# Performance work log

Hardware: AMD Instinct MI355X
Metric: run time of the kernel (lower is better)

## Reference

```python
import jax, jax.numpy as jnp
import numpy as np

N_ROWS = 8192
EMBED = 256


def setup_inputs() -> dict:
    key = jax.random.key(0)
    k1, k2, k3, k4, k5 = jax.random.split(key, 5)
    M = jax.random.normal(k1, (N_ROWS, EMBED), dtype=jnp.float32)
    N = jax.random.normal(k2, (N_ROWS, EMBED), dtype=jnp.float32)
    gate_w_weight = jax.random.normal(k3, (1, EMBED), dtype=jnp.float32) * (1.0 / np.sqrt(EMBED))
    gate_w_bias = jax.random.normal(k4, (1,), dtype=jnp.float32)
    gate_b = jax.random.normal(k5, (1,), dtype=jnp.float32)
    return {"M": M, "N": N, "gate_w_weight": gate_w_weight,
            "gate_w_bias": gate_w_bias, "gate_b": gate_b}


def reference(M, N, gate_w_weight, gate_w_bias, gate_b):
    # scores: [n, n] = N @ M^T
    mt = jnp.matmul(N, M.T)
    # zero the diagonal (mt - diag(diag(mt)))
    n = mt.shape[0]
    idx = jnp.arange(n)
    diag_zeroed = mt.at[idx, idx].set(0.0)
    attn = jax.nn.softmax(diag_zeroed, axis=-1)
    out_attn = jnp.matmul(attn, M)  # [n, d]
    # gate: Linear(d -> 1) + extra scalar bias, then sigmoid
    gate_tmp = jnp.matmul(out_attn, gate_w_weight.T) + gate_w_bias + gate_b  # [n, 1]
    gate = jax.nn.sigmoid(gate_tmp)
    boosted = out_attn * gate + N * (1.0 - gate)
    return boosted[:, None, None, :]  # [n, 1, 1, d]
```

## Files before the change

### kernel.cpp

```cpp
#include <hip/hip_runtime.h>
#include <math.h>

#define NR   8192
#define DIM  256
#define QBLK 32

using f32x4  = __attribute__((ext_vector_type(4))) float;
using s4v    = __attribute__((ext_vector_type(4))) short;
using s8v    = __attribute__((ext_vector_type(8))) short;
using bf16x8 = __attribute__((ext_vector_type(8))) short;
typedef _Float16 f16x8 __attribute__((ext_vector_type(8)));
typedef _Float16 f16x4 __attribute__((ext_vector_type(4)));

__device__ __forceinline__ short f2bf(float x){
  union{float f; unsigned u;} v; v.f = x;
  unsigned r = v.u + 0x7fffu + ((v.u >> 16) & 1u);
  return (short)(r >> 16);
}
__device__ __forceinline__ float bf2f(short s){
  union{unsigned u; float f;} v; v.u = ((unsigned)(unsigned short)s) << 16;
  return v.f;
}
__device__ __forceinline__ short f2h(float x){
  union{_Float16 h; short s;} c; c.h = (_Float16)x; return c.s;
}

#define SS_SHORTS 32768
#define WS_BYTES_NEEDED (128u * 32768u * 2u)

#define LDS6_SHORTS 65536

__device__ __forceinline__ void dma16(const short* g, short* l){
  __builtin_amdgcn_global_load_lds(
      (const __attribute__((address_space(1))) unsigned int*)g,
      (__attribute__((address_space(3))) unsigned int*)l, 16, 0, 0);
}

__launch_bounds__(256)
__global__ void precompute_ws(const float* __restrict__ Mp, short* __restrict__ ws)
{
  const int tid = threadIdx.x;
  const int bx  = blockIdx.x;
  const int ss  = bx >> 4;
  const int sub = bx & 15;
  const int fi  = sub*256 + tid;
  const int plane = fi >> 11;
  const int rest  = fi & 2047;
  const int p   = rest >> 10;
  const int cl  = rest & 1023;
  const int ch  = cl >> 6;
  const int l   = cl & 63;
  const int li  = l & 15, g = l >> 4;

  short v[8];
  if (plane == 0){
    const int kk = ch >> 1, n = ch & 1;
    const int row = ss*64 + p*32 + n*16 + li;
    const int d0  = kk*32 + g*8;
    const float* src = Mp + (size_t)row*DIM + d0;
    #pragma unroll
    for (int j = 0; j < 8; ++j) v[j] = f2h(src[j]);
  } else {
    const int u   = p*16 + ch;
    const int par = u >> 3;
    const int np  = u & 7;
    #pragma unroll
    for (int j = 0; j < 8; ++j){
      const int nf = 2*np + (j >> 2);
      const int jj = j & 3;
      const int row = ss*64 + par*16 + (l >> 4)*4 + jj;
      const int col = nf*16 + (l & 15);
      v[j] = f2h(Mp[(size_t)row*DIM + col]);
    }
  }
  s8v ov = {v[0],v[1],v[2],v[3],v[4],v[5],v[6],v[7]};
  *(s8v*)(ws + (size_t)ss*SS_SHORTS + plane*16384 + p*8192 + ch*512 + l*8) = ov;
}

__launch_bounds__(512, 2)
__global__ void attn_gate_v9(const float* __restrict__ Np,
                             const float* __restrict__ gw, const float* __restrict__ gwb,
                             const float* __restrict__ gb,
                             const short* __restrict__ ws, float* __restrict__ out)
{
  extern __shared__ short S_[];
  const int tid  = threadIdx.x;
  const int w    = tid >> 6;
  const int lane = tid & 63;
  const int g    = lane >> 4;
  const int li   = lane & 15;
  const int qsub = w & 1;
  const int par  = w >> 1;
  const int qb   = blockIdx.x * QBLK;
  const int fbase = w * 8;
  const int fadd  = (w < 4) ? 0 : 16384;

  f16x8 qh[8];
  {
    const float* qrow = Np + (size_t)(qb + qsub*16 + li) * DIM;
    #pragma unroll
    for (int kk = 0; kk < 8; ++kk){
      const int d0 = kk*32 + g*8;
      #pragma unroll
      for (int j = 0; j < 8; ++j)
        qh[kk][j] = (_Float16)qrow[d0 + j];
    }
  }

  f32x4 o[16];
  #pragma unroll
  for (int nf = 0; nf < 16; ++nf){ f32x4 z = {0.f,0.f,0.f,0.f}; o[nf] = z; }
  float m0 = -1e30f, l0 = 0.0f;

  const int p2 = par >> 1, n2 = par & 1;
  const int kfrag_off = p2*8192 + n2*512 + lane*8;

  #pragma unroll
  for (int i = 0; i < 8; ++i){
    const int f = fbase + i;
    dma16(ws + (size_t)f*512 + lane*8, S_ + f*512 + fadd);
  }
  __syncthreads();

  for (int ss = 0; ss < 128; ++ss){
    const size_t ssb = (size_t)ss * SS_SHORTS;
    const int cur = (ss & 1) * 16384;

    if (ss < 127){
      const int nxt = 16384 - cur;
      const size_t nsb = ssb + SS_SHORTS;
      #pragma unroll
      for (int i = 0; i < 8; ++i){
        const int f = fbase + i;
        dma16(ws + nsb + (size_t)f*512 + lane*8, S_ + f*512 + nxt + fadd);
      }
    }

    f32x4 sa0, sa1, sa2, sa3;
    { f32x4 z = {0.f,0.f,0.f,0.f}; sa0 = z; sa1 = z; sa2 = z; sa3 = z; }
    {
      const short* kbase = S_ + cur + kfrag_off;
      __builtin_amdgcn_s_setprio(1);
      #pragma unroll
      for (int kk = 0; kk < 2; ++kk){
        f16x8 bh = *(const f16x8*)(kbase + kk*1024);
        sa0 = __builtin_amdgcn_mfma_f32_16x16x32_f16(bh, qh[kk], sa0, 0, 0, 0);
      }
      #pragma unroll
      for (int kk = 2; kk < 4; ++kk){
        f16x8 bh = *(const f16x8*)(kbase + kk*1024);
        sa1 = __builtin_amdgcn_mfma_f32_16x16x32_f16(bh, qh[kk], sa1, 0, 0, 0);
      }
      #pragma unroll
      for (int kk = 4; kk < 6; ++kk){
        f16x8 bh = *(const f16x8*)(kbase + kk*1024);
        sa2 = __builtin_amdgcn_mfma_f32_16x16x32_f16(bh, qh[kk], sa2, 0, 0, 0);
      }
      #pragma unroll
      for (int kk = 6; kk < 8; ++kk){
        f16x8 bh = *(const f16x8*)(kbase + kk*1024);
        sa3 = __builtin_amdgcn_mfma_f32_16x16x32_f16(bh, qh[kk], sa3, 0, 0, 0);
      }
      __builtin_amdgcn_s_setprio(0);
    }

    const int kvb = ss*64 + par*16 + g*4;
    const int qg  = qb + qsub*16 + li;
    float s_[4];
    #pragma unroll
    for (int i = 0; i < 4; ++i){
      float sv = (sa0[i] + sa1[i]) + (sa2[i] + sa3[i]);
      if (kvb + i == qg) sv = 0.0f;
      s_[i] = sv;
    }
    const float lmax = fmaxf(fmaxf(s_[0], s_[1]), fmaxf(s_[2], s_[3]));
    float sc = 1.0f;
    if (__any((int)(lmax > m0 + 8.0f))){
      float t = lmax;
      t = fmaxf(t, __shfl_xor(t, 16));
      t = fmaxf(t, __shfl_xor(t, 32));
      const float mn = fmaxf(m0, t);
      sc = __expf(m0 - mn);
      m0 = mn;
      float scr[4];
      #pragma unroll
      for (int i = 0; i < 4; ++i) scr[i] = __shfl(sc, g*4 + i);
      #pragma unroll
      for (int nf = 0; nf < 16; ++nf)
        #pragma unroll
        for (int i = 0; i < 4; ++i) o[nf][i] *= scr[i];
    }

    float p_[4];
    #pragma unroll
    for (int i = 0; i < 4; ++i) p_[i] = __expf(s_[i] - m0);

    f16x4 pa4;
    pa4[0] = (_Float16)p_[0]; pa4[1] = (_Float16)p_[1];
    pa4[2] = (_Float16)p_[2]; pa4[3] = (_Float16)p_[3];
    {
      const short* vbase = S_ + 32768 + cur + par*4096 + lane*8;
      __builtin_amdgcn_s_setprio(1);
      #pragma unroll
      for (int np = 0; np < 8; ++np){
        f16x8 v8 = *(const f16x8*)(vbase + np*512);
        f16x4 lo = __builtin_shufflevector(v8, v8, 0, 1, 2, 3);
        f16x4 hi = __builtin_shufflevector(v8, v8, 4, 5, 6, 7);
        o[2*np]   = __builtin_amdgcn_mfma_f32_16x16x16f16(pa4, lo, o[2*np],   0, 0, 0);
        o[2*np+1] = __builtin_amdgcn_mfma_f32_16x16x16f16(pa4, hi, o[2*np+1], 0, 0, 0);
      }
      __builtin_amdgcn_s_setprio(0);
    }

    float ps = (p_[0] + p_[1]) + (p_[2] + p_[3]);
    ps += __shfl_xor(ps, 16);
    ps += __shfl_xor(ps, 32);
    l0 = l0*sc + ps;

    __syncthreads();
  }

  float mr[4], lr[4];
  #pragma unroll
  for (int i = 0; i < 4; ++i){
    mr[i] = __shfl(m0, g*4 + i);
    lr[i] = __shfl(l0, g*4 + i);
  }

  float* dump = (float*)S_;
  if (par > 0){
    float* dp = dump + (size_t)((par-1)*128 + qsub*64 + lane) * 72;
    #pragma unroll
    for (int i = 0; i < 4; ++i){ dp[i] = mr[i]; dp[4+i] = lr[i]; }
    #pragma unroll
    for (int nf = 0; nf < 16; ++nf)
      #pragma unroll
      for (int i = 0; i < 4; ++i) dp[8 + nf*4 + i] = o[nf][i];
  }
  __syncthreads();
  if (par == 0){
    #pragma unroll
    for (int pp = 0; pp < 3; ++pp){
      const float* dp = dump + (size_t)(pp*128 + qsub*64 + lane) * 72;
      float a[4], b[4];
      #pragma unroll
      for (int i = 0; i < 4; ++i){
        float mb = dp[i], lb = dp[4+i];
        float mm = fmaxf(mr[i], mb);
        a[i] = __expf(mr[i] - mm);
        b[i] = __expf(mb - mm);
        lr[i] = lr[i]*a[i] + lb*b[i];
        mr[i] = mm;
      }
      #pragma unroll
      for (int nf = 0; nf < 16; ++nf)
        #pragma unroll
        for (int i = 0; i < 4; ++i)
          o[nf][i] = o[nf][i]*a[i] + dp[8 + nf*4 + i]*b[i];
    }

    float inv[4];
    #pragma unroll
    for (int i = 0; i < 4; ++i) inv[i] = 1.0f / lr[i];
    #pragma unroll
    for (int nf = 0; nf < 16; ++nf)
      #pragma unroll
      for (int i = 0; i < 4; ++i) o[nf][i] *= inv[i];

    float acc[4] = {0.f, 0.f, 0.f, 0.f};
    #pragma unroll
    for (int nf = 0; nf < 16; ++nf){
      float wv = gw[nf*16 + li];
      #pragma unroll
      for (int i = 0; i < 4; ++i) acc[i] += o[nf][i] * wv;
    }
    const float bias = gwb[0] + gb[0];
    float gt[4];
    #pragma unroll
    for (int i = 0; i < 4; ++i){
      float x = acc[i];
      x += __shfl_xor(x, 1);
      x += __shfl_xor(x, 2);
      x += __shfl_xor(x, 4);
      x += __shfl_xor(x, 8);
      gt[i] = 1.0f / (1.0f + __expf(-(x + bias)));
    }
    #pragma unroll
    for (int i = 0; i < 4; ++i){
      const int grow = qb + qsub*16 + g*4 + i;
      const float* nrow = Np + (size_t)grow * DIM;
      float* orow = out + (size_t)grow * DIM;
      #pragma unroll
      for (int nf = 0; nf < 16; ++nf){
        const int col = nf*16 + li;
        float nv = nrow[col];
        orow[col] = o[nf][i]*gt[i] + nv*(1.0f - gt[i]);
      }
    }
  }
}

#define KH0 0
#define KH1 8448
#define KL0 16896
#define KL1 25344
#define MT0 33792
#define MT1 44032
#define PBO 54272
#define LDS0_SHORTS 56832

__launch_bounds__(256, 1)
__global__ void attn_gate_v0(const float* __restrict__ Mp, const float* __restrict__ Np,
                             const float* __restrict__ gw, const float* __restrict__ gwb,
                             const float* __restrict__ gb, float* __restrict__ out)
{
  extern __shared__ short S_[];
  const int tid  = threadIdx.x;
  const int w    = tid >> 6;
  const int lane = tid & 63;
  const int g    = lane >> 4;
  const int li   = lane & 15;
  const int qsub = w & 1;
  const int par  = w >> 1;
  const int qb   = blockIdx.x * QBLK;

  short* khp = S_ + (par ? KH1 : KH0);
  short* klp = S_ + (par ? KL1 : KL0);
  short* mtp = S_ + (par ? MT1 : MT0);
  short* pb  = S_ + PBO + w * 640;

  bf16x8 qh[8], ql[8];
  {
    const float* qrow = Np + (size_t)(qb + qsub*16 + li) * DIM;
    #pragma unroll
    for (int kk = 0; kk < 8; ++kk){
      const int d0 = kk*32 + g*8;
      #pragma unroll
      for (int j = 0; j < 8; ++j){
        float f = qrow[d0 + j];
        short h = f2bf(f);
        qh[kk][j] = h;
        ql[kk][j] = f2bf(f - bf2f(h));
      }
    }
  }

  f32x4 o[16];
  #pragma unroll
  for (int nf = 0; nf < 16; ++nf){ f32x4 z = {0.f,0.f,0.f,0.f}; o[nf] = z; }
  float m0[4], l0[4];
  #pragma unroll
  for (int i = 0; i < 4; ++i){ m0[i] = -1e30f; l0[i] = 0.0f; }

  const int NSS = NR / 64;
  for (int ss = 0; ss < NSS; ++ss){
    {
      const int r  = tid >> 2;
      const int cb = (tid & 3) << 6;
      const int p  = r >> 5;
      const int rr = r & 31;
      short* kh = S_ + (p ? KH1 : KH0) + rr*264 + cb;
      short* kl = S_ + (p ? KL1 : KL0) + rr*264 + cb;
      short* mt = S_ + (p ? MT1 : MT0) + rr;
      const float* src = Mp + (size_t)(ss*64 + r) * DIM + cb;
      #pragma unroll
      for (int c = 0; c < 64; c += 4){
        const float4 v = *(const float4*)(src + c);
        float fv[4] = {v.x, v.y, v.z, v.w};
        short h[4], lo[4];
        #pragma unroll
        for (int j = 0; j < 4; ++j){
          h[j]  = f2bf(fv[j]);
          lo[j] = f2bf(fv[j] - bf2f(h[j]));
          mt[(cb + c + j) * 40] = h[j];
        }
        s4v hv = {h[0], h[1], h[2], h[3]};
        s4v lv = {lo[0], lo[1], lo[2], lo[3]};
        *(s4v*)(kh + c) = hv;
        *(s4v*)(kl + c) = lv;
      }
    }
    __syncthreads();

    f32x4 sa[2];
    { f32x4 z = {0.f,0.f,0.f,0.f}; sa[0] = z; sa[1] = z; }
    #pragma unroll
    for (int kk = 0; kk < 8; ++kk){
      #pragma unroll
      for (int n = 0; n < 2; ++n){
        const int a = (n*16 + li)*264 + kk*32 + g*8;
        bf16x8 bh = *(const bf16x8*)(khp + a);
        bf16x8 bl = *(const bf16x8*)(klp + a);
        sa[n] = __builtin_amdgcn_mfma_f32_16x16x32_bf16(qh[kk], bh, sa[n], 0, 0, 0);
        sa[n] = __builtin_amdgcn_mfma_f32_16x16x32_bf16(qh[kk], bl, sa[n], 0, 0, 0);
        sa[n] = __builtin_amdgcn_mfma_f32_16x16x32_bf16(ql[kk], bh, sa[n], 0, 0, 0);
      }
    }

    const int kvb   = ss*64 + par*32;
    const int growb = qb + qsub*16 + g*4;
    float s_[2][4];
    #pragma unroll
    for (int n = 0; n < 2; ++n)
      #pragma unroll
      for (int i = 0; i < 4; ++i){
        float sv = sa[n][i];
        if (kvb + n*16 + li == growb + i) sv = 0.0f;
        s_[n][i] = sv;
      }
    float mn[4], sc[4], ps[4];
    bool need = false;
    #pragma unroll
    for (int i = 0; i < 4; ++i){
      float t = fmaxf(s_[0][i], s_[1][i]);
      t = fmaxf(t, __shfl_xor(t, 1));
      t = fmaxf(t, __shfl_xor(t, 2));
      t = fmaxf(t, __shfl_xor(t, 4));
      t = fmaxf(t, __shfl_xor(t, 8));
      mn[i] = fmaxf(m0[i], t);
      sc[i] = __expf(m0[i] - mn[i]);
      need |= (mn[i] != m0[i]);
      m0[i] = mn[i];
    }
    #pragma unroll
    for (int i = 0; i < 4; ++i) ps[i] = 0.0f;
    #pragma unroll
    for (int n = 0; n < 2; ++n)
      #pragma unroll
      for (int i = 0; i < 4; ++i){
        float p = __expf(s_[n][i] - mn[i]);
        ps[i] += p;
        pb[(g*4 + i)*40 + n*16 + li] = f2bf(p);
      }
    #pragma unroll
    for (int i = 0; i < 4; ++i){
      float t = ps[i];
      t += __shfl_xor(t, 1);
      t += __shfl_xor(t, 2);
      t += __shfl_xor(t, 4);
      t += __shfl_xor(t, 8);
      l0[i] = l0[i]*sc[i] + t;
    }
    if (__any((int)need)){
      #pragma unroll
      for (int nf = 0; nf < 16; ++nf)
        #pragma unroll
        for (int i = 0; i < 4; ++i) o[nf][i] *= sc[i];
    }

    bf16x8 pa = *(const bf16x8*)(pb + li*40 + g*8);
    #pragma unroll
    for (int nf = 0; nf < 16; ++nf){
      bf16x8 bv = *(const bf16x8*)(mtp + (nf*16 + li)*40 + g*8);
      o[nf] = __builtin_amdgcn_mfma_f32_16x16x32_bf16(pa, bv, o[nf], 0, 0, 0);
    }
    __syncthreads();
  }

  float* dump = (float*)S_;
  if (par == 1){
    float* dp = dump + (size_t)(qsub*64 + lane) * 72;
    #pragma unroll
    for (int i = 0; i < 4; ++i){ dp[i] = m0[i]; dp[4+i] = l0[i]; }
    #pragma unroll
    for (int nf = 0; nf < 16; ++nf)
      #pragma unroll
      for (int i = 0; i < 4; ++i) dp[8 + nf*4 + i] = o[nf][i];
  }
  __syncthreads();
  if (par == 0){
    const float* dp = dump + (size_t)(qsub*64 + lane) * 72;
    float a[4], b[4];
    #pragma unroll
    for (int i = 0; i < 4; ++i){
      float mb = dp[i], lb = dp[4+i];
      float mm = fmaxf(m0[i], mb);
      a[i] = __expf(m0[i] - mm);
      b[i] = __expf(mb - mm);
      l0[i] = l0[i]*a[i] + lb*b[i];
    }
    #pragma unroll
    for (int nf = 0; nf < 16; ++nf)
      #pragma unroll
      for (int i = 0; i < 4; ++i)
        o[nf][i] = o[nf][i]*a[i] + dp[8 + nf*4 + i]*b[i];

    float inv[4];
    #pragma unroll
    for (int i = 0; i < 4; ++i) inv[i] = 1.0f / l0[i];
    #pragma unroll
    for (int nf = 0; nf < 16; ++nf)
      #pragma unroll
      for (int i = 0; i < 4; ++i) o[nf][i] *= inv[i];

    float t[4] = {0.f, 0.f, 0.f, 0.f};
    #pragma unroll
    for (int nf = 0; nf < 16; ++nf){
      float wv = gw[nf*16 + li];
      #pragma unroll
      for (int i = 0; i < 4; ++i) t[i] += o[nf][i] * wv;
    }
    const float bias = gwb[0] + gb[0];
    float gt[4];
    #pragma unroll
    for (int i = 0; i < 4; ++i){
      float x = t[i];
      x += __shfl_xor(x, 1);
      x += __shfl_xor(x, 2);
      x += __shfl_xor(x, 4);
      x += __shfl_xor(x, 8);
      gt[i] = 1.0f / (1.0f + __expf(-(x + bias)));
    }
    #pragma unroll
    for (int i = 0; i < 4; ++i){
      const int grow = qb + qsub*16 + g*4 + i;
      const float* nrow = Np + (size_t)grow * DIM;
      float* orow = out + (size_t)grow * DIM;
      #pragma unroll
      for (int nf = 0; nf < 16; ++nf){
        const int col = nf*16 + li;
        float nv = nrow[col];
        orow[col] = o[nf][i]*gt[i] + nv*(1.0f - gt[i]);
      }
    }
  }
}

extern "C" void kernel_launch(void* const* d_in, const int* in_sizes, int n_in,
                              void* d_out, int out_size, void* d_ws, size_t ws_size,
                              hipStream_t stream)
{
  const float* Mp  = (const float*)d_in[0];
  const float* Np  = (const float*)d_in[1];
  const float* gw  = (const float*)d_in[2];
  const float* gwb = (const float*)d_in[3];
  const float* gb  = (const float*)d_in[4];
  float* out = (float*)d_out;

  if (ws_size >= (size_t)WS_BYTES_NEEDED){
    short* ws = (short*)d_ws;
    precompute_ws<<<128*16, 256, 0, stream>>>(Mp, ws);
    const size_t shmem = (size_t)LDS6_SHORTS * sizeof(short);
    (void)hipFuncSetAttribute((const void*)attn_gate_v9,
                        hipFuncAttributeMaxDynamicSharedMemorySize, (int)shmem);
    attn_gate_v9<<<NR / QBLK, 512, shmem, stream>>>(Np, gw, gwb, gb, ws, out);
  } else {
    const size_t shmem = (size_t)LDS0_SHORTS * sizeof(short);
    (void)hipFuncSetAttribute((const void*)attn_gate_v0,
                        hipFuncAttributeMaxDynamicSharedMemorySize, (int)shmem);
    attn_gate_v0<<<NR / QBLK, 256, shmem, stream>>>(Mp, Np, gw, gwb, gb, out);
  }
}
```

Baseline: 175.5 us.

## Defer PV MFMA by one tile to overlap with next QK MFMA

Software-pipelines the attention loop: the P·V MFMAs for the previous key tile are issued right after the current tile's Q·K MFMAs, so the softmax/exp work no longer sits between dependent matrix ops. V tiles move to a triple-buffered LDS rotation, and K stays double-buffered, so LDS per block grows. A final epilogue drains the last PV step. The deferred PV is added after any running-max rescale of the accumulator, which may slightly change numerics when the max updates.

```diff
diff --git a/kernel.cpp b/kernel.cpp
--- a/kernel.cpp
+++ b/kernel.cpp
@@ -28,7 +28,7 @@
 #define SS_SHORTS 32768
 #define WS_BYTES_NEEDED (128u * 32768u * 2u)
 
-#define LDS6_SHORTS 65536
+#define LDS8_SHORTS 81920
 
 __device__ __forceinline__ void dma16(const short* g, short* l){
   __builtin_amdgcn_global_load_lds(
@@ -78,10 +78,10 @@
 }
 
 __launch_bounds__(512, 2)
-__global__ void attn_gate_v9(const float* __restrict__ Np,
-                             const float* __restrict__ gw, const float* __restrict__ gwb,
-                             const float* __restrict__ gb,
-                             const short* __restrict__ ws, float* __restrict__ out)
+__global__ void attn_gate_v10(const float* __restrict__ Np,
+                              const float* __restrict__ gw, const float* __restrict__ gwb,
+                              const float* __restrict__ gb,
+                              const short* __restrict__ ws, float* __restrict__ out)
 {
   extern __shared__ short S_[];
   const int tid  = threadIdx.x;
@@ -93,7 +93,7 @@
   const int par  = w >> 1;
   const int qb   = blockIdx.x * QBLK;
   const int fbase = w * 8;
-  const int fadd  = (w < 4) ? 0 : 16384;
+  const bool isK  = (w < 4);
 
   f16x8 qh[8];
   {
@@ -115,51 +115,78 @@
   const int p2 = par >> 1, n2 = par & 1;
   const int kfrag_off = p2*8192 + n2*512 + lane*8;
 
-  #pragma unroll
-  for (int i = 0; i < 8; ++i){
-    const int f = fbase + i;
-    dma16(ws + (size_t)f*512 + lane*8, S_ + f*512 + fadd);
+  int khc = 0;
+  int vtr = 65536;
+  int vtc = 32768;
+  int vtf = 49152;
+
+  {
+    const int ldst = isK ? 0 : (32768 - 16384);
+    #pragma unroll
+    for (int i = 0; i < 8; ++i){
+      const int f = fbase + i;
+      dma16(ws + (size_t)f*512 + lane*8, S_ + ldst + f*512);
+    }
   }
   __syncthreads();
+
+  f16x4 paP;
+  paP[0] = (_Float16)0.f; paP[1] = (_Float16)0.f;
+  paP[2] = (_Float16)0.f; paP[3] = (_Float16)0.f;
 
   for (int ss = 0; ss < 128; ++ss){
     const size_t ssb = (size_t)ss * SS_SHORTS;
-    const int cur = (ss & 1) * 16384;
 
     if (ss < 127){
-      const int nxt = 16384 - cur;
       const size_t nsb = ssb + SS_SHORTS;
+      const int ldst = isK ? (khc ^ 16384) : (vtf - 16384);
       #pragma unroll
       for (int i = 0; i < 8; ++i){
         const int f = fbase + i;
-        dma16(ws + nsb + (size_t)f*512 + lane*8, S_ + f*512 + nxt + fadd);
+        dma16(ws + nsb + (size_t)f*512 + lane*8, S_ + ldst + f*512);
       }
     }
 
     f32x4 sa0, sa1, sa2, sa3;
     { f32x4 z = {0.f,0.f,0.f,0.f}; sa0 = z; sa1 = z; sa2 = z; sa3 = z; }
     {
-      const short* kbase = S_ + cur + kfrag_off;
+      const short* kbase = S_ + khc + kfrag_off;
       __builtin_amdgcn_s_setprio(1);
-      #pragma unroll
-      for (int kk = 0; kk < 2; ++kk){
-        f16x8 bh = *(const f16x8*)(kbase + kk*1024);
-        sa0 = __builtin_amdgcn_mfma_f32_16x16x32_f16(bh, qh[kk], sa0, 0, 0, 0);
-      }
-      #pragma unroll
-      for (int kk = 2; kk < 4; ++kk){
-        f16x8 bh = *(const f16x8*)(kbase + kk*1024);
-        sa1 = __builtin_amdgcn_mfma_f32_16x16x32_f16(bh, qh[kk], sa1, 0, 0, 0);
-      }
-      #pragma unroll
-      for (int kk = 4; kk < 6; ++kk){
-        f16x8 bh = *(const f16x8*)(kbase + kk*1024);
-        sa2 = __builtin_amdgcn_mfma_f32_16x16x32_f16(bh, qh[kk], sa2, 0, 0, 0);
-      }
-      #pragma unroll
-      for (int kk = 6; kk < 8; ++kk){
-        f16x8 bh = *(const f16x8*)(kbase + kk*1024);
-        sa3 = __builtin_amdgcn_mfma_f32_16x16x32_f16(bh, qh[kk], sa3, 0, 0, 0);
+      {
+        f16x8 b0 = *(const f16x8*)(kbase);
+        f16x8 b1 = *(const f16x8*)(kbase + 1024);
+        sa0 = __builtin_amdgcn_mfma_f32_16x16x32_f16(b0, qh[0], sa0, 0, 0, 0);
+        sa0 = __builtin_amdgcn_mfma_f32_16x16x32_f16(b1, qh[1], sa0, 0, 0, 0);
+      }
+      {
+        f16x8 b2 = *(const f16x8*)(kbase + 2048);
+        f16x8 b3 = *(const f16x8*)(kbase + 3072);
+        sa1 = __builtin_amdgcn_mfma_f32_16x16x32_f16(b2, qh[2], sa1, 0, 0, 0);
+        sa1 = __builtin_amdgcn_mfma_f32_16x16x32_f16(b3, qh[3], sa1, 0, 0, 0);
+      }
+      {
+        f16x8 b4 = *(const f16x8*)(kbase + 4096);
+        f16x8 b5 = *(const f16x8*)(kbase + 5120);
+        sa2 = __builtin_amdgcn_mfma_f32_16x16x32_f16(b4, qh[4], sa2, 0, 0, 0);
+        sa2 = __builtin_amdgcn_mfma_f32_16x16x32_f16(b5, qh[5], sa2, 0, 0, 0);
+      }
+      {
+        f16x8 b6 = *(const f16x8*)(kbase + 6144);
+        f16x8 b7 = *(const f16x8*)(kbase + 7168);
+        sa3 = __builtin_amdgcn_mfma_f32_16x16x32_f16(b6, qh[6], sa3, 0, 0, 0);
+        sa3 = __builtin_amdgcn_mfma_f32_16x16x32_f16(b7, qh[7], sa3, 0, 0, 0);
+      }
+
+      if (ss > 0){
+        const short* vbase = S_ + vtr + par*4096 + lane*8;
+        #pragma unroll
+        for (int np = 0; np < 8; ++np){
+          f16x8 v8 = *(const f16x8*)(vbase + np*512);
+          f16x4 lo = __builtin_shufflevector(v8, v8, 0, 1, 2, 3);
+          f16x4 hi = __builtin_shufflevector(v8, v8, 4, 5, 6, 7);
+          o[2*np]   = __builtin_amdgcn_mfma_f32_16x16x16f16(paP, lo, o[2*np],   0, 0, 0);
+          o[2*np+1] = __builtin_amdgcn_mfma_f32_16x16x16f16(paP, hi, o[2*np+1], 0, 0, 0);
+        }
       }
       __builtin_amdgcn_s_setprio(0);
     }
@@ -194,23 +221,8 @@
     float p_[4];
     #pragma unroll
     for (int i = 0; i < 4; ++i) p_[i] = __expf(s_[i] - m0);
-
-    f16x4 pa4;
-    pa4[0] = (_Float16)p_[0]; pa4[1] = (_Float16)p_[1];
-    pa4[2] = (_Float16)p_[2]; pa4[3] = (_Float16)p_[3];
-    {
-      const short* vbase = S_ + 32768 + cur + par*4096 + lane*8;
-      __builtin_amdgcn_s_setprio(1);
-      #pragma unroll
-      for (int np = 0; np < 8; ++np){
-        f16x8 v8 = *(const f16x8*)(vbase + np*512);
-        f16x4 lo = __builtin_shufflevector(v8, v8, 0, 1, 2, 3);
-        f16x4 hi = __builtin_shufflevector(v8, v8, 4, 5, 6, 7);
-        o[2*np]   = __builtin_amdgcn_mfma_f32_16x16x16f16(pa4, lo, o[2*np],   0, 0, 0);
-        o[2*np+1] = __builtin_amdgcn_mfma_f32_16x16x16f16(pa4, hi, o[2*np+1], 0, 0, 0);
-      }
-      __builtin_amdgcn_s_setprio(0);
-    }
+    paP[0] = (_Float16)p_[0]; paP[1] = (_Float16)p_[1];
+    paP[2] = (_Float16)p_[2]; paP[3] = (_Float16)p_[3];
 
     float ps = (p_[0] + p_[1]) + (p_[2] + p_[3]);
     ps += __shfl_xor(ps, 16);
@@ -218,7 +230,23 @@
     l0 = l0*sc + ps;
 
     __syncthreads();
-  }
+
+    const int t = vtr; vtr = vtc; vtc = vtf; vtf = t;
+    khc ^= 16384;
+  }
+
+  {
+    const short* vbase = S_ + vtr + par*4096 + lane*8;
+    #pragma unroll
+    for (int np = 0; np < 8; ++np){
+      f16x8 v8 = *(const f16x8*)(vbase + np*512);
+      f16x4 lo = __builtin_shufflevector(v8, v8, 0, 1, 2, 3);
+      f16x4 hi = __builtin_shufflevector(v8, v8, 4, 5, 6, 7);
+      o[2*np]   = __builtin_amdgcn_mfma_f32_16x16x16f16(paP, lo, o[2*np],   0, 0, 0);
+      o[2*np+1] = __builtin_amdgcn_mfma_f32_16x16x16f16(paP, hi, o[2*np+1], 0, 0, 0);
+    }
+  }
+  __syncthreads();
 
   float mr[4], lr[4];
   #pragma unroll
@@ -540,10 +568,10 @@
   if (ws_size >= (size_t)WS_BYTES_NEEDED){
     short* ws = (short*)d_ws;
     precompute_ws<<<128*16, 256, 0, stream>>>(Mp, ws);
-    const size_t shmem = (size_t)LDS6_SHORTS * sizeof(short);
-    (void)hipFuncSetAttribute((const void*)attn_gate_v9,
+    const size_t shmem = (size_t)LDS8_SHORTS * sizeof(short);
+    (void)hipFuncSetAttribute((const void*)attn_gate_v10,
                         hipFuncAttributeMaxDynamicSharedMemorySize, (int)shmem);
-    attn_gate_v9<<<NR / QBLK, 512, shmem, stream>>>(Np, gw, gwb, gb, ws, out);
+    attn_gate_v10<<<NR / QBLK, 512, shmem, stream>>>(Np, gw, gwb, gb, ws, out);
   } else {
     const size_t shmem = (size_t)LDS0_SHORTS * sizeof(short);
     (void)hipFuncSetAttribute((const void*)attn_gate_v0,
```

Result: faster. 169.5 us (-3.4%).
